# Kernel optimization log

Measured on AMD Instinct MI355X. Metric: run time of the kernel, lower is better.

Reference implementation:

```python
import jax, jax.numpy as jnp
import numpy as np

TEMPERATURE = 0.1
NEG_INF = -1e30


def setup_inputs() -> dict:
    key = jax.random.key(0)
    ks = jax.random.split(key, 8)
    T, B, D = 2048, 16, 256
    inp = {
        'q1': jax.random.normal(ks[0], (T, B, D), dtype=jnp.float32),
        'k2': jax.random.normal(ks[1], (T, B, D), dtype=jnp.float32),
        'q2': jax.random.normal(ks[2], (T, B, D), dtype=jnp.float32),
        'k1': jax.random.normal(ks[3], (T, B, D), dtype=jnp.float32),
        'mask_q1': jnp.ones((B, T), dtype=bool),
        'mask_q2': jnp.ones((B, T), dtype=bool),
        'len_q1': jax.random.randint(ks[4], (B,), 0, T, dtype=jnp.int32),
        'len_k2': jax.random.randint(ks[5], (B,), 0, T, dtype=jnp.int32),
        'len_q2': jax.random.randint(ks[6], (B,), 0, T, dtype=jnp.int32),
        'len_k1': jax.random.randint(ks[7], (B,), 0, T, dtype=jnp.int32),
    }
    return inp


def _compute_loss(pred, target, len_pred, len_target):
    # pred, target: (T, B, D) -> (B, T, D)
    pred = jnp.transpose(pred, (1, 0, 2))
    target = jnp.transpose(target, (1, 0, 2))
    B, T, _ = pred.shape
    min_l = jnp.minimum(len_pred, len_target)  # (B,)

    # Batched truncated matmul realized as full matmul + column masking.
    logits = jnp.einsum('btd,bsd->bts', pred, target) / TEMPERATURE  # (B, T, T)
    idx = jnp.arange(T)
    col_valid = idx[None, None, :] < min_l[:, None, None]
    logits = jnp.where(col_valid, logits, NEG_INF)

    # Cross-entropy with labels = arange(min_l): loss_i = lse_i - logits[i, i]
    lse = jax.nn.logsumexp(logits, axis=-1)                 # (B, T)
    diag = jnp.diagonal(logits, axis1=1, axis2=2)           # (B, T)
    row_loss = lse - diag

    row_valid = idx[None, :] < min_l[:, None]               # (B, T)
    denom = jnp.maximum(min_l, 1).astype(pred.dtype)
    per_sample = jnp.sum(jnp.where(row_valid, row_loss, 0.0), axis=1) / denom

    valid = min_l > 0
    n_valid = jnp.sum(valid.astype(pred.dtype))
    total = jnp.sum(jnp.where(valid, per_sample, 0.0))
    return jnp.where(n_valid > 0, total / jnp.maximum(n_valid, 1.0), 0.0)


def reference(q1, k2, q2, k1, mask_q1, mask_q2, len_q1, len_k2, len_q2, len_k1):
    # masks are unused in the original math (kept for interface fidelity)
    loss_a = _compute_loss(q1, k2, len_q1, len_k2)
    loss_b = _compute_loss(q2, k1, len_q2, len_k1)
    return (loss_a + loss_b) / 2
```

## Files before the change

kernel.cpp:

```cpp
#include <hip/hip_runtime.h>
#include <hip/hip_bf16.h>
#include <cmath>

#define T_DIM 2048
#define B_DIM 16
#define D_DIM 256
#define BD (B_DIM * D_DIM)
#define BM 256
#define BN 64
#define NS 4
#define CHUNK (T_DIM / NS)
#define NEG_INF_F (-1e30f)

typedef __attribute__((ext_vector_type(8))) short bf16x8;
typedef __attribute__((ext_vector_type(8))) unsigned short ushort8;
typedef __attribute__((ext_vector_type(4))) float f32x4;

static __device__ __forceinline__ ushort f2bf(float f) {
    union { float f; unsigned int u; } x; x.f = f;
    unsigned int r = (x.u + 0x7FFFu + ((x.u >> 16) & 1u)) >> 16;
    return (ushort)r;
}

static __device__ __forceinline__ void gload_lds16(const ushort* g, ushort* l) {
    __builtin_amdgcn_global_load_lds(
        (const __attribute__((address_space(1))) unsigned int*)g,
        (__attribute__((address_space(3))) unsigned int*)l,
        16, 0, 0);
}

__global__ __launch_bounds__(256) void convert_kernel(
    const float* __restrict__ q1, const float* __restrict__ k2,
    const float* __restrict__ q2, const float* __restrict__ k1,
    const int* __restrict__ lq1, const int* __restrict__ lk2,
    const int* __restrict__ lq2, const int* __restrict__ lk1,
    ushort* __restrict__ wsbf)
{
    const int idx    = blockIdx.x * 256 + threadIdx.x;
    const int tensor = idx >> 20;
    const int rem    = idx & 1048575;
    const int t      = rem >> 9;
    const int r2     = rem & 511;
    const int b      = r2 >> 5;
    const int d8     = (r2 & 31) * 8;
    const int m = (tensor < 2) ? min(lq1[b], lk2[b]) : min(lq2[b], lk1[b]);
    if (t >= m) return;

    const float* src = (tensor == 0) ? q1 : (tensor == 1) ? k2 : (tensor == 2) ? q2 : k1;
    const float scale = (tensor == 0 || tensor == 2) ? 10.0f : 1.0f;
    const size_t off = (size_t)t * BD + (size_t)b * D_DIM + d8;
    const float4 v0 = *reinterpret_cast<const float4*>(&src[off]);
    const float4 v1 = *reinterpret_cast<const float4*>(&src[off + 4]);
    ushort8 h;
    h[0] = f2bf(v0.x * scale); h[1] = f2bf(v0.y * scale);
    h[2] = f2bf(v0.z * scale); h[3] = f2bf(v0.w * scale);
    h[4] = f2bf(v1.x * scale); h[5] = f2bf(v1.y * scale);
    h[6] = f2bf(v1.z * scale); h[7] = f2bf(v1.w * scale);
    const size_t TBD = (size_t)T_DIM * BD;
    ushort* dst = &wsbf[(size_t)tensor * TBD + (size_t)t * BD + (size_t)b * D_DIM
                        + (d8 ^ ((t & 15) << 3))];
    *reinterpret_cast<ushort8*>(dst) = h;
}

__global__ __launch_bounds__(512) void partial_lse_bf_kernel(
    const ushort* __restrict__ wsbf,
    const int* __restrict__ len_q1, const int* __restrict__ len_k2,
    const int* __restrict__ len_q2, const int* __restrict__ len_k1,
    float2* __restrict__ partial, float* __restrict__ diag)
{
    const int pair = blockIdx.z / NS;
    const int sc   = blockIdx.z % NS;
    const int b    = blockIdx.y;
    const int t0   = blockIdx.x * BM;

    const int lp = (pair == 0) ? len_q1[b] : len_q2[b];
    const int lt = (pair == 0) ? len_k2[b] : len_k1[b];
    const int m  = min(lp, lt);
    const int s_start = sc * CHUNK;
    if (t0 >= m || s_start >= m) return;
    const int s_hi = min(m, s_start + CHUNK);
    const int pb = pair * B_DIM + b;

    const size_t TBD = (size_t)T_DIM * BD;
    const ushort* pred = wsbf + (size_t)(pair ? 2 : 0) * TBD;
    const ushort* targ = wsbf + (size_t)(pair ? 3 : 1) * TBD;

    __shared__ ushort tl[2][BN * 256];

    const int tid = threadIdx.x;
    const int w   = tid >> 6;
    const int l   = tid & 63;
    const int c   = l & 15;
    const int g   = l >> 4;

    #pragma unroll
    for (int q = 0; q < 4; ++q) {
        const int r = 8 * w + 2 * q + (l >> 5);
        const ushort* gp = &targ[(size_t)(s_start + r) * BD + (size_t)b * D_DIM + (l & 31) * 8];
        gload_lds16(gp, &tl[0][(4 * w + q) * 512]);
    }

    bf16x8 afrag[2][8];
    #pragma unroll
    for (int i = 0; i < 2; ++i) {
        const ushort* base = &pred[(size_t)(t0 + 32 * w + 16 * i + c) * BD + (size_t)b * D_DIM];
        #pragma unroll
        for (int kk = 0; kk < 8; ++kk) {
            const int d = g * 8 + kk * 32;
            afrag[i][kk] = *reinterpret_cast<const bf16x8*>(&base[d ^ (c << 3)]);
        }
    }

    float tmax[2][4], tsum[2][4], dg[2][4];
    #pragma unroll
    for (int i = 0; i < 2; ++i)
        #pragma unroll
        for (int rr = 0; rr < 4; ++rr) {
            tmax[i][rr] = NEG_INF_F; tsum[i][rr] = 0.0f; dg[i][rr] = NEG_INF_F;
        }

    __syncthreads();
    int cur = 0;

    for (int s0 = s_start; s0 < s_hi; s0 += BN) {
        if (s0 + BN < s_hi) {
            const int nxt = cur ^ 1;
            #pragma unroll
            for (int q = 0; q < 4; ++q) {
                const int r = 8 * w + 2 * q + (l >> 5);
                const ushort* gp = &targ[(size_t)(s0 + BN + r) * BD + (size_t)b * D_DIM + (l & 31) * 8];
                gload_lds16(gp, &tl[nxt][(4 * w + q) * 512]);
            }
        }

        f32x4 acc[2][4];
        #pragma unroll
        for (int i = 0; i < 2; ++i)
            #pragma unroll
            for (int j = 0; j < 4; ++j)
                acc[i][j] = (f32x4){0.f, 0.f, 0.f, 0.f};

        const ushort* buf = tl[cur];
        #pragma unroll
        for (int kk = 0; kk < 8; ++kk) {
            bf16x8 bfrag[4];
            #pragma unroll
            for (int j = 0; j < 4; ++j) {
                const int r = 16 * j + c;
                const int d = g * 8 + kk * 32;
                bfrag[j] = *reinterpret_cast<const bf16x8*>(&buf[(r << 8) + (d ^ (c << 3))]);
            }
            #pragma unroll
            for (int i = 0; i < 2; ++i)
                #pragma unroll
                for (int j = 0; j < 4; ++j)
                    acc[i][j] = __builtin_amdgcn_mfma_f32_16x16x32_bf16(
                        afrag[i][kk], bfrag[j], acc[i][j], 0, 0, 0);
        }

        #pragma unroll
        for (int i = 0; i < 2; ++i) {
            #pragma unroll
            for (int rr = 0; rr < 4; ++rr) {
                const int trow = t0 + 32 * w + 16 * i + 4 * g + rr;
                float lg[4];
                float cmax = NEG_INF_F;
                #pragma unroll
                for (int j = 0; j < 4; ++j) {
                    const int s = s0 + 16 * j + c;
                    float v = acc[i][j][rr];
                    v = (s < m) ? v : NEG_INF_F;
                    if (s == trow) dg[i][rr] = v;
                    lg[j] = v;
                    cmax = fmaxf(cmax, v);
                }
                const float nmax = fmaxf(tmax[i][rr], cmax);
                const float add = __expf(lg[0] - nmax) + __expf(lg[1] - nmax)
                                + __expf(lg[2] - nmax) + __expf(lg[3] - nmax);
                tsum[i][rr] = tsum[i][rr] * __expf(tmax[i][rr] - nmax) + add;
                tmax[i][rr] = nmax;
            }
        }

        __syncthreads();
        cur ^= 1;
    }

    const bool own_diag = (t0 >= s_start) && (t0 + BM <= s_start + CHUNK);
    #pragma unroll
    for (int i = 0; i < 2; ++i) {
        #pragma unroll
        for (int rr = 0; rr < 4; ++rr) {
            float M = tmax[i][rr], S = tsum[i][rr];
            #pragma unroll
            for (int msk = 1; msk < 16; msk <<= 1) {
                const float Mo = __shfl_xor(M, msk, 64);
                const float So = __shfl_xor(S, msk, 64);
                const float nM = fmaxf(M, Mo);
                S = S * __expf(M - nM) + So * __expf(Mo - nM);
                M = nM;
            }
            float d = dg[i][rr];
            #pragma unroll
            for (int msk = 1; msk < 16; msk <<= 1)
                d = fmaxf(d, __shfl_xor(d, msk, 64));
            if (c == 0) {
                const int trow = t0 + 32 * w + 16 * i + 4 * g + rr;
                partial[((size_t)(pb << 11) + trow) * NS + sc] = make_float2(M, S);
                if (own_diag) diag[(pb << 11) + trow] = d;
            }
        }
    }
}

__global__ __launch_bounds__(256) void partial_lse_f32_kernel(
    const float* __restrict__ q1, const float* __restrict__ k2,
    const float* __restrict__ q2, const float* __restrict__ k1,
    const int* __restrict__ len_q1, const int* __restrict__ len_k2,
    const int* __restrict__ len_q2, const int* __restrict__ len_k1,
    float2* __restrict__ partial, float* __restrict__ diag,
    int chunk, int ns)
{
    const int pair = blockIdx.z / ns;
    const int sc   = blockIdx.z % ns;
    const int b    = blockIdx.y;
    const int t0   = blockIdx.x * 128;

    const float* pred = (pair == 0) ? q1 : q2;
    const float* targ = (pair == 0) ? k2 : k1;
    const int lp = (pair == 0) ? len_q1[b] : len_q2[b];
    const int lt = (pair == 0) ? len_k2[b] : len_k1[b];
    const int m  = min(lp, lt);
    const int s_start = sc * chunk;
    if (t0 >= m || s_start >= m) return;
    const int s_hi = min(m, s_start + chunk);
    const int pb = pair * B_DIM + b;

    __shared__ ushort tlf[BN * 256];

    const int tid = threadIdx.x;
    const int w   = tid >> 6;
    const int l   = tid & 63;
    const int c   = l & 15;
    const int g   = l >> 4;

    bf16x8 afrag[2][8];
    #pragma unroll
    for (int i = 0; i < 2; ++i) {
        const float* base = &pred[(size_t)(t0 + 32 * w + 16 * i + c) * BD + (size_t)b * D_DIM];
        #pragma unroll
        for (int kk = 0; kk < 8; ++kk) {
            const int d = g * 8 + kk * 32;
            const float4 v0 = *reinterpret_cast<const float4*>(base + d);
            const float4 v1 = *reinterpret_cast<const float4*>(base + d + 4);
            bf16x8 av;
            av[0] = (short)f2bf(v0.x * 10.f); av[1] = (short)f2bf(v0.y * 10.f);
            av[2] = (short)f2bf(v0.z * 10.f); av[3] = (short)f2bf(v0.w * 10.f);
            av[4] = (short)f2bf(v1.x * 10.f); av[5] = (short)f2bf(v1.y * 10.f);
            av[6] = (short)f2bf(v1.z * 10.f); av[7] = (short)f2bf(v1.w * 10.f);
            afrag[i][kk] = av;
        }
    }

    float tmax[2][4], tsum[2][4], dg[2][4];
    #pragma unroll
    for (int i = 0; i < 2; ++i)
        #pragma unroll
        for (int rr = 0; rr < 4; ++rr) {
            tmax[i][rr] = NEG_INF_F; tsum[i][rr] = 0.0f; dg[i][rr] = NEG_INF_F;
        }

    for (int s0 = s_start; s0 < s_hi; s0 += BN) {
        __syncthreads();
        #pragma unroll
        for (int v = 0; v < 16; ++v) {
            const int f  = v * 256 + tid;
            const int r  = f >> 6;
            const int d0 = (f & 63) * 4;
            const float4 vv = *reinterpret_cast<const float4*>(
                &targ[(size_t)(s0 + r) * BD + (size_t)b * D_DIM + d0]);
            ushort4 h;
            h.x = f2bf(vv.x); h.y = f2bf(vv.y); h.z = f2bf(vv.z); h.w = f2bf(vv.w);
            *reinterpret_cast<ushort4*>(&tlf[(r << 8) + (d0 ^ ((r & 15) << 3))]) = h;
        }
        __syncthreads();

        f32x4 acc[2][4];
        #pragma unroll
        for (int i = 0; i < 2; ++i)
            #pragma unroll
            for (int j = 0; j < 4; ++j)
                acc[i][j] = (f32x4){0.f, 0.f, 0.f, 0.f};

        #pragma unroll
        for (int kk = 0; kk < 8; ++kk) {
            bf16x8 bfrag[4];
            #pragma unroll
            for (int j = 0; j < 4; ++j) {
                const int r = 16 * j + c;
                const int d = g * 8 + kk * 32;
                bfrag[j] = *reinterpret_cast<const bf16x8*>(&tlf[(r << 8) + (d ^ (c << 3))]);
            }
            #pragma unroll
            for (int i = 0; i < 2; ++i)
                #pragma unroll
                for (int j = 0; j < 4; ++j)
                    acc[i][j] = __builtin_amdgcn_mfma_f32_16x16x32_bf16(
                        afrag[i][kk], bfrag[j], acc[i][j], 0, 0, 0);
        }

        #pragma unroll
        for (int i = 0; i < 2; ++i) {
            #pragma unroll
            for (int rr = 0; rr < 4; ++rr) {
                const int trow = t0 + 32 * w + 16 * i + 4 * g + rr;
                float lg[4];
                float cmax = NEG_INF_F;
                #pragma unroll
                for (int j = 0; j < 4; ++j) {
                    const int s = s0 + 16 * j + c;
                    float v = acc[i][j][rr];
                    v = (s < m) ? v : NEG_INF_F;
                    if (s == trow) dg[i][rr] = v;
                    lg[j] = v;
                    cmax = fmaxf(cmax, v);
                }
                const float nmax = fmaxf(tmax[i][rr], cmax);
                const float add = __expf(lg[0] - nmax) + __expf(lg[1] - nmax)
                                + __expf(lg[2] - nmax) + __expf(lg[3] - nmax);
                tsum[i][rr] = tsum[i][rr] * __expf(tmax[i][rr] - nmax) + add;
                tmax[i][rr] = nmax;
            }
        }
    }

    const bool own_diag = (t0 >= s_start) && (t0 + 128 <= s_start + chunk);
    #pragma unroll
    for (int i = 0; i < 2; ++i) {
        #pragma unroll
        for (int rr = 0; rr < 4; ++rr) {
            float M = tmax[i][rr], S = tsum[i][rr];
            #pragma unroll
            for (int msk = 1; msk < 16; msk <<= 1) {
                const float Mo = __shfl_xor(M, msk, 64);
                const float So = __shfl_xor(S, msk, 64);
                const float nM = fmaxf(M, Mo);
                S = S * __expf(M - nM) + So * __expf(Mo - nM);
                M = nM;
            }
            float d = dg[i][rr];
            #pragma unroll
            for (int msk = 1; msk < 16; msk <<= 1)
                d = fmaxf(d, __shfl_xor(d, msk, 64));
            if (c == 0) {
                const int trow = t0 + 32 * w + 16 * i + 4 * g + rr;
                partial[((size_t)(pb << 11) + trow) * ns + sc] = make_float2(M, S);
                if (own_diag) diag[(pb << 11) + trow] = d;
            }
        }
    }
}

__global__ __launch_bounds__(256) void combine_kernel(
    const int* __restrict__ len_q1, const int* __restrict__ len_k2,
    const int* __restrict__ len_q2, const int* __restrict__ len_k1,
    const float2* __restrict__ partial, const float* __restrict__ diag,
    float* __restrict__ per_sample, int chunk, int ns)
{
    const int pb   = blockIdx.x;
    const int pair = pb >> 4;
    const int b    = pb & 15;
    const int lp = (pair == 0) ? len_q1[b] : len_q2[b];
    const int lt = (pair == 0) ? len_k2[b] : len_k1[b];
    const int m  = min(lp, lt);

    float local = 0.0f;
    if (m > 0) {
        const int nch = (m + chunk - 1) / chunk;
        for (int t = threadIdx.x; t < m; t += 256) {
            float M = NEG_INF_F, S = 0.0f;
            for (int sc = 0; sc < nch; ++sc) {
                const float2 p = partial[((size_t)(pb << 11) + t) * ns + sc];
                const float nM = fmaxf(M, p.x);
                S = S * __expf(M - nM) + p.y * __expf(p.x - nM);
                M = nM;
            }
            local += (__logf(S) + M) - diag[(pb << 11) + t];
        }
    }

    __shared__ float ws4[4];
    #pragma unroll
    for (int msk = 1; msk < 64; msk <<= 1)
        local += __shfl_xor(local, msk, 64);
    if ((threadIdx.x & 63) == 0) ws4[threadIdx.x >> 6] = local;
    __syncthreads();
    if (threadIdx.x == 0) {
        const float tot = ws4[0] + ws4[1] + ws4[2] + ws4[3];
        per_sample[pb] = (m > 0) ? (tot / (float)m) : 0.0f;
    }
}

__global__ void finalize_kernel(
    const int* __restrict__ len_q1, const int* __restrict__ len_k2,
    const int* __restrict__ len_q2, const int* __restrict__ len_k1,
    const float* __restrict__ per_sample, float* __restrict__ out)
{
    if (threadIdx.x != 0 || blockIdx.x != 0) return;
    float losses[2];
    #pragma unroll
    for (int p = 0; p < 2; ++p) {
        float tot = 0.0f, nv = 0.0f;
        for (int b = 0; b < B_DIM; ++b) {
            const int lp = (p == 0) ? len_q1[b] : len_q2[b];
            const int lt = (p == 0) ? len_k2[b] : len_k1[b];
            const int mm = min(lp, lt);
            if (mm > 0) { tot += per_sample[p * B_DIM + b]; nv += 1.0f; }
        }
        losses[p] = (nv > 0.0f) ? (tot / nv) : 0.0f;
    }
    out[0] = 0.5f * (losses[0] + losses[1]);
}

extern "C" void kernel_launch(void* const* d_in, const int* in_sizes, int n_in,
                              void* d_out, int out_size, void* d_ws, size_t ws_size,
                              hipStream_t stream) {
    const float* q1 = (const float*)d_in[0];
    const float* k2 = (const float*)d_in[1];
    const float* q2 = (const float*)d_in[2];
    const float* k1 = (const float*)d_in[3];
    const int* lq1 = (const int*)d_in[6];
    const int* lk2 = (const int*)d_in[7];
    const int* lq2 = (const int*)d_in[8];
    const int* lk1 = (const int*)d_in[9];
    float* out = (float*)d_out;

    const size_t TBD  = (size_t)T_DIM * BD;
    const size_t rows = (size_t)2 * B_DIM * T_DIM;
    const size_t bfbytes = 4 * TBD * sizeof(ushort);
    const size_t need_pre = bfbytes + rows * NS * sizeof(float2) + rows * sizeof(float) + 256;

    if (ws_size >= need_pre) {
        ushort* wsbf       = (ushort*)d_ws;
        float2* partial    = (float2*)((char*)d_ws + bfbytes);
        float*  diag       = (float*)((char*)partial + rows * NS * sizeof(float2));
        float*  per_sample = diag + rows;

        convert_kernel<<<16384, 256, 0, stream>>>(q1, k2, q2, k1, lq1, lk2, lq2, lk1, wsbf);

        dim3 gridA(T_DIM / BM, B_DIM, 2 * NS);
        partial_lse_bf_kernel<<<gridA, 512, 0, stream>>>(
            wsbf, lq1, lk2, lq2, lk1, partial, diag);

        combine_kernel<<<32, 256, 0, stream>>>(
            lq1, lk2, lq2, lk1, partial, diag, per_sample, CHUNK, NS);
        finalize_kernel<<<1, 64, 0, stream>>>(lq1, lk2, lq2, lk1, per_sample, out);
    } else {
        int ns = 8;
        while (ns > 1) {
            const size_t need = rows * ns * sizeof(float2) + rows * sizeof(float) + 256;
            if (need <= ws_size) break;
            ns >>= 1;
        }
        const int chunk = T_DIM / ns;
        float2* partial    = (float2*)d_ws;
        float*  diag       = (float*)((char*)d_ws + rows * ns * sizeof(float2));
        float*  per_sample = diag + rows;

        dim3 gridA(T_DIM / 128, B_DIM, 2 * ns);
        partial_lse_f32_kernel<<<gridA, 256, 0, stream>>>(
            q1, k2, q2, k1, lq1, lk2, lq2, lk1, partial, diag, chunk, ns);

        combine_kernel<<<32, 256, 0, stream>>>(
            lq1, lk2, lq2, lk1, partial, diag, per_sample, chunk, ns);
        finalize_kernel<<<1, 64, 0, stream>>>(lq1, lk2, lq2, lk1, per_sample, out);
    }
}
```

Measured before the change: 77.69 us.

## Shrink bf16 LSE tiles, raise key-split count, and use exp2 with log2-scaled logits

The main bf16 path now uses 128-row tiles with 32-column key blocks and 256-thread blocks. It splits the key dimension into up to 16 chunks, chosen at runtime from workspace size, to launch many more blocks and balance the work that variable sequence lengths leave uneven. The temperature scale is folded together with log2(e) into the converted queries so the softmax can use exp2 directly, and the result is converted back with ln2 in the combine step. In exchange there are more partial LSE entries to write and merge, and smaller MFMA tiles with less reuse per LDS load.

New measurement: 106.6 us. 37.2% more time.

```diff
diff --git a/kernel.cpp b/kernel.cpp
--- a/kernel.cpp
+++ b/kernel.cpp
@@ -6,11 +6,11 @@
 #define B_DIM 16
 #define D_DIM 256
 #define BD (B_DIM * D_DIM)
-#define BM 256
-#define BN 64
-#define NS 4
-#define CHUNK (T_DIM / NS)
+#define BM 128
+#define BN 32
 #define NEG_INF_F (-1e30f)
+#define SCALE_LOG2 14.4269504088896f
+#define LN2F 0.6931471805599453f
 
 typedef __attribute__((ext_vector_type(8))) short bf16x8;
 typedef __attribute__((ext_vector_type(8))) unsigned short ushort8;
@@ -47,7 +47,7 @@
     if (t >= m) return;
 
     const float* src = (tensor == 0) ? q1 : (tensor == 1) ? k2 : (tensor == 2) ? q2 : k1;
-    const float scale = (tensor == 0 || tensor == 2) ? 10.0f : 1.0f;
+    const float scale = (tensor == 0 || tensor == 2) ? SCALE_LOG2 : 1.0f;
     const size_t off = (size_t)t * BD + (size_t)b * D_DIM + d8;
     const float4 v0 = *reinterpret_cast<const float4*>(&src[off]);
     const float4 v1 = *reinterpret_cast<const float4*>(&src[off + 4]);
@@ -62,23 +62,24 @@
     *reinterpret_cast<ushort8*>(dst) = h;
 }
 
-__global__ __launch_bounds__(512) void partial_lse_bf_kernel(
+__global__ __launch_bounds__(256) void partial_lse_bf_kernel(
     const ushort* __restrict__ wsbf,
     const int* __restrict__ len_q1, const int* __restrict__ len_k2,
     const int* __restrict__ len_q2, const int* __restrict__ len_k1,
-    float2* __restrict__ partial, float* __restrict__ diag)
+    float2* __restrict__ partial, float* __restrict__ diag,
+    int chunk, int ns)
 {
-    const int pair = blockIdx.z / NS;
-    const int sc   = blockIdx.z % NS;
+    const int pair = blockIdx.z / ns;
+    const int sc   = blockIdx.z % ns;
     const int b    = blockIdx.y;
     const int t0   = blockIdx.x * BM;
 
     const int lp = (pair == 0) ? len_q1[b] : len_q2[b];
     const int lt = (pair == 0) ? len_k2[b] : len_k1[b];
     const int m  = min(lp, lt);
-    const int s_start = sc * CHUNK;
+    const int s_start = sc * chunk;
     if (t0 >= m || s_start >= m) return;
-    const int s_hi = min(m, s_start + CHUNK);
+    const int s_hi = min(m, s_start + chunk);
     const int pb = pair * B_DIM + b;
 
     const size_t TBD = (size_t)T_DIM * BD;
@@ -93,17 +94,20 @@
     const int c   = l & 15;
     const int g   = l >> 4;
 
-    #pragma unroll
-    for (int q = 0; q < 4; ++q) {
-        const int r = 8 * w + 2 * q + (l >> 5);
-        const ushort* gp = &targ[(size_t)(s_start + r) * BD + (size_t)b * D_DIM + (l & 31) * 8];
-        gload_lds16(gp, &tl[0][(4 * w + q) * 512]);
+    {
+        #pragma unroll
+        for (int q = 0; q < 4; ++q) {
+            const int r = 8 * w + 2 * q + (l >> 5);
+            const ushort* gp = &targ[(size_t)(s_start + r) * BD + (size_t)b * D_DIM + (l & 31) * 8];
+            gload_lds16(gp, &tl[0][(4 * w + q) * 512]);
+        }
     }
 
     bf16x8 afrag[2][8];
     #pragma unroll
     for (int i = 0; i < 2; ++i) {
-        const ushort* base = &pred[(size_t)(t0 + 32 * w + 16 * i + c) * BD + (size_t)b * D_DIM];
+        const int trow = t0 + 32 * w + 16 * i + c;
+        const ushort* base = &pred[(size_t)trow * BD + (size_t)b * D_DIM];
         #pragma unroll
         for (int kk = 0; kk < 8; ++kk) {
             const int d = g * 8 + kk * 32;
@@ -133,6 +137,152 @@
             }
         }
 
+        f32x4 acc[2][2];
+        #pragma unroll
+        for (int i = 0; i < 2; ++i)
+            #pragma unroll
+            for (int j = 0; j < 2; ++j)
+                acc[i][j] = (f32x4){0.f, 0.f, 0.f, 0.f};
+
+        const ushort* buf = tl[cur];
+        #pragma unroll
+        for (int kk = 0; kk < 8; ++kk) {
+            bf16x8 bfrag[2];
+            #pragma unroll
+            for (int j = 0; j < 2; ++j) {
+                const int r = 16 * j + c;
+                const int d = g * 8 + kk * 32;
+                bfrag[j] = *reinterpret_cast<const bf16x8*>(&buf[(r << 8) + (d ^ (c << 3))]);
+            }
+            #pragma unroll
+            for (int i = 0; i < 2; ++i)
+                #pragma unroll
+                for (int j = 0; j < 2; ++j)
+                    acc[i][j] = __builtin_amdgcn_mfma_f32_16x16x32_bf16(
+                        afrag[i][kk], bfrag[j], acc[i][j], 0, 0, 0);
+        }
+
+        #pragma unroll
+        for (int i = 0; i < 2; ++i) {
+            #pragma unroll
+            for (int rr = 0; rr < 4; ++rr) {
+                const int trow = t0 + 32 * w + 16 * i + 4 * g + rr;
+                const int s0c  = s0 + c;
+                float v0 = (s0c      < m) ? acc[i][0][rr] : NEG_INF_F;
+                float v1 = (s0c + 16 < m) ? acc[i][1][rr] : NEG_INF_F;
+                if (s0c      == trow) dg[i][rr] = v0;
+                if (s0c + 16 == trow) dg[i][rr] = v1;
+                const float cmax = fmaxf(v0, v1);
+                const float nmax = fmaxf(tmax[i][rr], cmax);
+                const float add  = exp2f(v0 - nmax) + exp2f(v1 - nmax);
+                tsum[i][rr] = tsum[i][rr] * exp2f(tmax[i][rr] - nmax) + add;
+                tmax[i][rr] = nmax;
+            }
+        }
+
+        __syncthreads();
+        cur ^= 1;
+    }
+
+    const bool own_diag = (t0 >= s_start) && (t0 + BM <= s_start + chunk);
+    #pragma unroll
+    for (int i = 0; i < 2; ++i) {
+        #pragma unroll
+        for (int rr = 0; rr < 4; ++rr) {
+            float M = tmax[i][rr], S = tsum[i][rr];
+            #pragma unroll
+            for (int msk = 1; msk < 16; msk <<= 1) {
+                const float Mo = __shfl_xor(M, msk, 64);
+                const float So = __shfl_xor(S, msk, 64);
+                const float nM = fmaxf(M, Mo);
+                S = S * exp2f(M - nM) + So * exp2f(Mo - nM);
+                M = nM;
+            }
+            float d = dg[i][rr];
+            #pragma unroll
+            for (int msk = 1; msk < 16; msk <<= 1)
+                d = fmaxf(d, __shfl_xor(d, msk, 64));
+            if (c == 0) {
+                const int trow = t0 + 32 * w + 16 * i + 4 * g + rr;
+                partial[((size_t)(pb << 11) + trow) * ns + sc] = make_float2(M, S);
+                if (own_diag) diag[(pb << 11) + trow] = d;
+            }
+        }
+    }
+}
+
+__global__ __launch_bounds__(256) void partial_lse_f32_kernel(
+    const float* __restrict__ q1, const float* __restrict__ k2,
+    const float* __restrict__ q2, const float* __restrict__ k1,
+    const int* __restrict__ len_q1, const int* __restrict__ len_k2,
+    const int* __restrict__ len_q2, const int* __restrict__ len_k1,
+    float2* __restrict__ partial, float* __restrict__ diag,
+    int chunk, int ns)
+{
+    const int pair = blockIdx.z / ns;
+    const int sc   = blockIdx.z % ns;
+    const int b    = blockIdx.y;
+    const int t0   = blockIdx.x * 128;
+
+    const float* pred = (pair == 0) ? q1 : q2;
+    const float* targ = (pair == 0) ? k2 : k1;
+    const int lp = (pair == 0) ? len_q1[b] : len_q2[b];
+    const int lt = (pair == 0) ? len_k2[b] : len_k1[b];
+    const int m  = min(lp, lt);
+    const int s_start = sc * chunk;
+    if (t0 >= m || s_start >= m) return;
+    const int s_hi = min(m, s_start + chunk);
+    const int pb = pair * B_DIM + b;
+
+    __shared__ ushort tlf[64 * 256];
+
+    const int tid = threadIdx.x;
+    const int w   = tid >> 6;
+    const int l   = tid & 63;
+    const int c   = l & 15;
+    const int g   = l >> 4;
+
+    bf16x8 afrag[2][8];
+    #pragma unroll
+    for (int i = 0; i < 2; ++i) {
+        const float* base = &pred[(size_t)(t0 + 32 * w + 16 * i + c) * BD + (size_t)b * D_DIM];
+        #pragma unroll
+        for (int kk = 0; kk < 8; ++kk) {
+            const int d = g * 8 + kk * 32;
+            const float4 v0 = *reinterpret_cast<const float4*>(base + d);
+            const float4 v1 = *reinterpret_cast<const float4*>(base + d + 4);
+            bf16x8 av;
+            av[0] = (short)f2bf(v0.x * SCALE_LOG2); av[1] = (short)f2bf(v0.y * SCALE_LOG2);
+            av[2] = (short)f2bf(v0.z * SCALE_LOG2); av[3] = (short)f2bf(v0.w * SCALE_LOG2);
+            av[4] = (short)f2bf(v1.x * SCALE_LOG2); av[5] = (short)f2bf(v1.y * SCALE_LOG2);
+            av[6] = (short)f2bf(v1.z * SCALE_LOG2); av[7] = (short)f2bf(v1.w * SCALE_LOG2);
+            afrag[i][kk] = av;
+        }
+    }
+
+    float tmax[2][4], tsum[2][4], dg[2][4];
+    #pragma unroll
+    for (int i = 0; i < 2; ++i)
+        #pragma unroll
+        for (int rr = 0; rr < 4; ++rr) {
+            tmax[i][rr] = NEG_INF_F; tsum[i][rr] = 0.0f; dg[i][rr] = NEG_INF_F;
+        }
+
+    for (int s0 = s_start; s0 < s_hi; s0 += 64) {
+        __syncthreads();
+        #pragma unroll
+        for (int v = 0; v < 16; ++v) {
+            const int f  = v * 256 + tid;
+            const int r  = f >> 6;
+            const int d0 = (f & 63) * 4;
+            const float4 vv = *reinterpret_cast<const float4*>(
+                &targ[(size_t)(s0 + r) * BD + (size_t)b * D_DIM + d0]);
+            ushort4 hh;
+            hh.x = f2bf(vv.x); hh.y = f2bf(vv.y); hh.z = f2bf(vv.z); hh.w = f2bf(vv.w);
+            *reinterpret_cast<ushort4*>(&tlf[(r << 8) + (d0 ^ ((r & 15) << 3))]) = hh;
+        }
+        __syncthreads();
+
         f32x4 acc[2][4];
         #pragma unroll
         for (int i = 0; i < 2; ++i)
@@ -140,7 +290,6 @@
             for (int j = 0; j < 4; ++j)
                 acc[i][j] = (f32x4){0.f, 0.f, 0.f, 0.f};
 
-        const ushort* buf = tl[cur];
         #pragma unroll
         for (int kk = 0; kk < 8; ++kk) {
             bf16x8 bfrag[4];
@@ -148,7 +297,7 @@
             for (int j = 0; j < 4; ++j) {
                 const int r = 16 * j + c;
                 const int d = g * 8 + kk * 32;
-                bfrag[j] = *reinterpret_cast<const bf16x8*>(&buf[(r << 8) + (d ^ (c << 3))]);
+                bfrag[j] = *reinterpret_cast<const bf16x8*>(&tlf[(r << 8) + (d ^ (c << 3))]);
             }
             #pragma unroll
             for (int i = 0; i < 2; ++i)
@@ -175,18 +324,15 @@
                     cmax = fmaxf(cmax, v);
                 }
                 const float nmax = fmaxf(tmax[i][rr], cmax);
-                const float add = __expf(lg[0] - nmax) + __expf(lg[1] - nmax)
-                                + __expf(lg[2] - nmax) + __expf(lg[3] - nmax);
-                tsum[i][rr] = tsum[i][rr] * __expf(tmax[i][rr] - nmax) + add;
+                const float add = exp2f(lg[0] - nmax) + exp2f(lg[1] - nmax)
+                                + exp2f(lg[2] - nmax) + exp2f(lg[3] - nmax);
+                tsum[i][rr] = tsum[i][rr] * exp2f(tmax[i][rr] - nmax) + add;
                 tmax[i][rr] = nmax;
             }
         }
-
-        __syncthreads();
-        cur ^= 1;
-    }
-
-    const bool own_diag = (t0 >= s_start) && (t0 + BM <= s_start + CHUNK);
+    }
+
+    const bool own_diag = (t0 >= s_start) && (t0 + 128 <= s_start + chunk);
     #pragma unroll
     for (int i = 0; i < 2; ++i) {
         #pragma unroll
@@ -197,155 +343,7 @@
                 const float Mo = __shfl_xor(M, msk, 64);
                 const float So = __shfl_xor(S, msk, 64);
                 const float nM = fmaxf(M, Mo);
-                S = S * __expf(M - nM) + So * __expf(Mo - nM);
-                M = nM;
-            }
-            float d = dg[i][rr];
-            #pragma unroll
-            for (int msk = 1; msk < 16; msk <<= 1)
-                d = fmaxf(d, __shfl_xor(d, msk, 64));
-            if (c == 0) {
-                const int trow = t0 + 32 * w + 16 * i + 4 * g + rr;
-                partial[((size_t)(pb << 11) + trow) * NS + sc] = make_float2(M, S);
-                if (own_diag) diag[(pb << 11) + trow] = d;
-            }
-        }
-    }
-}
-
-__global__ __launch_bounds__(256) void partial_lse_f32_kernel(
-    const float* __restrict__ q1, const float* __restrict__ k2,
-    const float* __restrict__ q2, const float* __restrict__ k1,
-    const int* __restrict__ len_q1, const int* __restrict__ len_k2,
-    const int* __restrict__ len_q2, const int* __restrict__ len_k1,
-    float2* __restrict__ partial, float* __restrict__ diag,
-    int chunk, int ns)
-{
-    const int pair = blockIdx.z / ns;
-    const int sc   = blockIdx.z % ns;
-    const int b    = blockIdx.y;
-    const int t0   = blockIdx.x * 128;
-
-    const float* pred = (pair == 0) ? q1 : q2;
-    const float* targ = (pair == 0) ? k2 : k1;
-    const int lp = (pair == 0) ? len_q1[b] : len_q2[b];
-    const int lt = (pair == 0) ? len_k2[b] : len_k1[b];
-    const int m  = min(lp, lt);
-    const int s_start = sc * chunk;
-    if (t0 >= m || s_start >= m) return;
-    const int s_hi = min(m, s_start + chunk);
-    const int pb = pair * B_DIM + b;
-
-    __shared__ ushort tlf[BN * 256];
-
-    const int tid = threadIdx.x;
-    const int w   = tid >> 6;
-    const int l   = tid & 63;
-    const int c   = l & 15;
-    const int g   = l >> 4;
-
-    bf16x8 afrag[2][8];
-    #pragma unroll
-    for (int i = 0; i < 2; ++i) {
-        const float* base = &pred[(size_t)(t0 + 32 * w + 16 * i + c) * BD + (size_t)b * D_DIM];
-        #pragma unroll
-        for (int kk = 0; kk < 8; ++kk) {
-            const int d = g * 8 + kk * 32;
-            const float4 v0 = *reinterpret_cast<const float4*>(base + d);
-            const float4 v1 = *reinterpret_cast<const float4*>(base + d + 4);
-            bf16x8 av;
-            av[0] = (short)f2bf(v0.x * 10.f); av[1] = (short)f2bf(v0.y * 10.f);
-            av[2] = (short)f2bf(v0.z * 10.f); av[3] = (short)f2bf(v0.w * 10.f);
-            av[4] = (short)f2bf(v1.x * 10.f); av[5] = (short)f2bf(v1.y * 10.f);
-            av[6] = (short)f2bf(v1.z * 10.f); av[7] = (short)f2bf(v1.w * 10.f);
-            afrag[i][kk] = av;
-        }
-    }
-
-    float tmax[2][4], tsum[2][4], dg[2][4];
-    #pragma unroll
-    for (int i = 0; i < 2; ++i)
-        #pragma unroll
-        for (int rr = 0; rr < 4; ++rr) {
-            tmax[i][rr] = NEG_INF_F; tsum[i][rr] = 0.0f; dg[i][rr] = NEG_INF_F;
-        }
-
-    for (int s0 = s_start; s0 < s_hi; s0 += BN) {
-        __syncthreads();
-        #pragma unroll
-        for (int v = 0; v < 16; ++v) {
-            const int f  = v * 256 + tid;
-            const int r  = f >> 6;
-            const int d0 = (f & 63) * 4;
-            const float4 vv = *reinterpret_cast<const float4*>(
-                &targ[(size_t)(s0 + r) * BD + (size_t)b * D_DIM + d0]);
-            ushort4 h;
-            h.x = f2bf(vv.x); h.y = f2bf(vv.y); h.z = f2bf(vv.z); h.w = f2bf(vv.w);
-            *reinterpret_cast<ushort4*>(&tlf[(r << 8) + (d0 ^ ((r & 15) << 3))]) = h;
-        }
-        __syncthreads();
-
-        f32x4 acc[2][4];
-        #pragma unroll
-        for (int i = 0; i < 2; ++i)
-            #pragma unroll
-            for (int j = 0; j < 4; ++j)
-                acc[i][j] = (f32x4){0.f, 0.f, 0.f, 0.f};
-
-        #pragma unroll
-        for (int kk = 0; kk < 8; ++kk) {
-            bf16x8 bfrag[4];
-            #pragma unroll
-            for (int j = 0; j < 4; ++j) {
-                const int r = 16 * j + c;
-                const int d = g * 8 + kk * 32;
-                bfrag[j] = *reinterpret_cast<const bf16x8*>(&tlf[(r << 8) + (d ^ (c << 3))]);
-            }
-            #pragma unroll
-            for (int i = 0; i < 2; ++i)
-                #pragma unroll
-                for (int j = 0; j < 4; ++j)
-                    acc[i][j] = __builtin_amdgcn_mfma_f32_16x16x32_bf16(
-                        afrag[i][kk], bfrag[j], acc[i][j], 0, 0, 0);
-        }
-
-        #pragma unroll
-        for (int i = 0; i < 2; ++i) {
-            #pragma unroll
-            for (int rr = 0; rr < 4; ++rr) {
-                const int trow = t0 + 32 * w + 16 * i + 4 * g + rr;
-                float lg[4];
-                float cmax = NEG_INF_F;
-                #pragma unroll
-                for (int j = 0; j < 4; ++j) {
-                    const int s = s0 + 16 * j + c;
-                    float v = acc[i][j][rr];
-                    v = (s < m) ? v : NEG_INF_F;
-                    if (s == trow) dg[i][rr] = v;
-                    lg[j] = v;
-                    cmax = fmaxf(cmax, v);
-                }
-                const float nmax = fmaxf(tmax[i][rr], cmax);
-                const float add = __expf(lg[0] - nmax) + __expf(lg[1] - nmax)
-                                + __expf(lg[2] - nmax) + __expf(lg[3] - nmax);
-                tsum[i][rr] = tsum[i][rr] * __expf(tmax[i][rr] - nmax) + add;
-                tmax[i][rr] = nmax;
-            }
-        }
-    }
-
-    const bool own_diag = (t0 >= s_start) && (t0 + 128 <= s_start + chunk);
-    #pragma unroll
-    for (int i = 0; i < 2; ++i) {
-        #pragma unroll
-        for (int rr = 0; rr < 4; ++rr) {
-            float M = tmax[i][rr], S = tsum[i][rr];
-            #pragma unroll
-            for (int msk = 1; msk < 16; msk <<= 1) {
-                const float Mo = __shfl_xor(M, msk, 64);
-                const float So = __shfl_xor(S, msk, 64);
-                const float nM = fmaxf(M, Mo);
-                S = S * __expf(M - nM) + So * __expf(Mo - nM);
+                S = S * exp2f(M - nM) + So * exp2f(Mo - nM);
                 M = nM;
             }
             float d = dg[i][rr];
@@ -365,7 +363,7 @@
     const int* __restrict__ len_q1, const int* __restrict__ len_k2,
     const int* __restrict__ len_q2, const int* __restrict__ len_k1,
     const float2* __restrict__ partial, const float* __restrict__ diag,
-    float* __restrict__ per_sample, int chunk, int ns)
+    float* __restrict__ per_sample, int chunk, int stride)
 {
     const int pb   = blockIdx.x;
     const int pair = pb >> 4;
@@ -379,13 +377,13 @@
         const int nch = (m + chunk - 1) / chunk;
         for (int t = threadIdx.x; t < m; t += 256) {
             float M = NEG_INF_F, S = 0.0f;
-            for (int sc = 0; sc < nch; ++sc) {
-                const float2 p = partial[((size_t)(pb << 11) + t) * ns + sc];
+            for (int e = 0; e < nch; ++e) {
+                const float2 p = partial[((size_t)(pb << 11) + t) * stride + e];
                 const float nM = fmaxf(M, p.x);
-                S = S * __expf(M - nM) + p.y * __expf(p.x - nM);
+                S = S * exp2f(M - nM) + p.y * exp2f(p.x - nM);
                 M = nM;
             }
-            local += (__logf(S) + M) - diag[(pb << 11) + t];
+            local += LN2F * ((__log2f(S) + M) - diag[(pb << 11) + t]);
         }
     }
 
@@ -438,41 +436,49 @@
     const size_t TBD  = (size_t)T_DIM * BD;
     const size_t rows = (size_t)2 * B_DIM * T_DIM;
     const size_t bfbytes = 4 * TBD * sizeof(ushort);
-    const size_t need_pre = bfbytes + rows * NS * sizeof(float2) + rows * sizeof(float) + 256;
+
+    int ns = 16;
+    while (ns > 4) {
+        const size_t need = bfbytes + rows * ns * sizeof(float2) + rows * sizeof(float) + 256;
+        if (need <= ws_size) break;
+        ns >>= 1;
+    }
+    const size_t need_pre = bfbytes + rows * ns * sizeof(float2) + rows * sizeof(float) + 256;
 
     if (ws_size >= need_pre) {
+        const int chunk = T_DIM / ns;
         ushort* wsbf       = (ushort*)d_ws;
         float2* partial    = (float2*)((char*)d_ws + bfbytes);
-        float*  diag       = (float*)((char*)partial + rows * NS * sizeof(float2));
+        float*  diag       = (float*)((char*)partial + rows * ns * sizeof(float2));
         float*  per_sample = diag + rows;
 
         convert_kernel<<<16384, 256, 0, stream>>>(q1, k2, q2, k1, lq1, lk2, lq2, lk1, wsbf);
 
-        dim3 gridA(T_DIM / BM, B_DIM, 2 * NS);
-        partial_lse_bf_kernel<<<gridA, 512, 0, stream>>>(
-            wsbf, lq1, lk2, lq2, lk1, partial, diag);
-
-        combine_kernel<<<32, 256, 0, stream>>>(
-            lq1, lk2, lq2, lk1, partial, diag, per_sample, CHUNK, NS);
-        finalize_kernel<<<1, 64, 0, stream>>>(lq1, lk2, lq2, lk1, per_sample, out);
-    } else {
-        int ns = 8;
-        while (ns > 1) {
-            const size_t need = rows * ns * sizeof(float2) + rows * sizeof(float) + 256;
-            if (need <= ws_size) break;
-            ns >>= 1;
-        }
-        const int chunk = T_DIM / ns;
-        float2* partial    = (float2*)d_ws;
-        float*  diag       = (float*)((char*)d_ws + rows * ns * sizeof(float2));
-        float*  per_sample = diag + rows;
-
-        dim3 gridA(T_DIM / 128, B_DIM, 2 * ns);
-        partial_lse_f32_kernel<<<gridA, 256, 0, stream>>>(
-            q1, k2, q2, k1, lq1, lk2, lq2, lk1, partial, diag, chunk, ns);
+        dim3 gridA(T_DIM / BM, B_DIM, 2 * ns);
+        partial_lse_bf_kernel<<<gridA, 256, 0, stream>>>(
+            wsbf, lq1, lk2, lq2, lk1, partial, diag, chunk, ns);
 
         combine_kernel<<<32, 256, 0, stream>>>(
             lq1, lk2, lq2, lk1, partial, diag, per_sample, chunk, ns);
         finalize_kernel<<<1, 64, 0, stream>>>(lq1, lk2, lq2, lk1, per_sample, out);
-    }
-}
+    } else {
+        int nsf = 8;
+        while (nsf > 1) {
+            const size_t need = rows * nsf * sizeof(float2) + rows * sizeof(float) + 256;
+            if (need <= ws_size) break;
+            nsf >>= 1;
+        }
+        const int chunk = T_DIM / nsf;
+        float2* partial    = (float2*)d_ws;
+        float*  diag       = (float*)((char*)d_ws + rows * nsf * sizeof(float2));
+        float*  per_sample = diag + rows;
+
+        dim3 gridA(T_DIM / 128, B_DIM, 2 * nsf);
+        partial_lse_f32_kernel<<<gridA, 256, 0, stream>>>(
+            q1, k2, q2, k1, lq1, lk2, lq2, lk1, partial, diag, chunk, nsf);
+
+        combine_kernel<<<32, 256, 0, stream>>>(
+            lq1, lk2, lq2, lk1, partial, diag, per_sample, chunk, nsf);
+        finalize_kernel<<<1, 64, 0, stream>>>(lq1, lk2, lq2, lk1, per_sample, out);
+    }
+}
```
